# Kernel tuning notes

Hardware: AMD Instinct MI355X
Metric: run time of the kernel (lower is better)

The kernel has to match this reference:

```python
import jax, jax.numpy as jnp
import numpy as np

WS = 7            # window size
NUM_HEADS = 16
DIM = 512
B_ = 4096         # num_windows * batch
NW = 1024         # windows per image
N = WS * WS


def _relative_position_index(ws=WS):
    # static int index table, computed exactly as in the torch module
    coords = np.stack(np.meshgrid(np.arange(ws), np.arange(ws), indexing='ij'))  # (2, ws, ws)
    coords = coords.reshape(2, -1)                                               # (2, N)
    rel = coords[:, :, None] - coords[:, None, :]                                # (2, N, N)
    rel = rel.transpose(1, 2, 0).astype(np.int64)                                # (N, N, 2)
    rel[:, :, 0] += ws - 1
    rel[:, :, 1] += ws - 1
    rel[:, :, 0] *= 2 * ws - 1
    return jnp.asarray(rel.sum(-1))                                              # (N, N)


def setup_inputs() -> dict:
    key = jax.random.key(0)
    ks = jax.random.split(key, 12)
    C = DIM
    std = 0.02
    inp = {
        'local_features': jax.random.normal(ks[0], (B_, N, C), jnp.float32),
        'global_features': jax.random.normal(ks[1], (B_, N, C), jnp.float32),
        'mask': jnp.zeros((NW, N, N), jnp.float32),  # 0/-inf shifted-window mask (all-visible here)
        'bias_table': std * jax.random.normal(ks[2], ((2 * WS - 1) * (2 * WS - 1), NUM_HEADS), jnp.float32),
        'Wk': std * jax.random.normal(ks[3], (C, C), jnp.float32),
        'bk': jnp.zeros((C,), jnp.float32),
        'Wq': std * jax.random.normal(ks[4], (C, C), jnp.float32),
        'bq': jnp.zeros((C,), jnp.float32),
        'Wv': std * jax.random.normal(ks[5], (C, C), jnp.float32),
        'bv': jnp.zeros((C,), jnp.float32),
        'Wp': std * jax.random.normal(ks[6], (C, C), jnp.float32),
        'bp': jnp.zeros((C,), jnp.float32),
    }
    return inp


def reference(local_features, global_features, mask, bias_table,
              Wk, bk, Wq, bq, Wv, bv, Wp, bp):
    Bw, n, C = local_features.shape
    h = NUM_HEADS
    d = C // h
    scale = d ** -0.5

    def heads(x, W, b):
        # torch Linear: x @ W.T + b ; then (B_, N, h, d) -> (B_, h, N, d)
        y = jnp.einsum('bnc,oc->bno', x, W) + b
        return y.reshape(Bw, n, h, d).transpose(0, 2, 1, 3)

    k = heads(local_features, Wk, bk)
    q = heads(global_features, Wq, bq) * scale
    v = heads(local_features, Wv, bv)

    attn = jnp.einsum('bhnd,bhmd->bhnm', q, k)                    # (B_, h, N, N)

    idx = _relative_position_index()                               # (N, N) static
    rpb = bias_table[idx]                                          # (N, N, h)
    attn = attn + rpb.transpose(2, 0, 1)[None]                     # add (1, h, N, N)

    nW = mask.shape[0]
    attn = attn.reshape(Bw // nW, nW, h, n, n) + mask[None, :, None]
    attn = attn.reshape(Bw, h, n, n)
    attn = jax.nn.softmax(attn, axis=-1)

    x = jnp.einsum('bhnm,bhmd->bnhd', attn, v).reshape(Bw, n, C)
    x = jnp.einsum('bnc,oc->bno', x, Wp) + bp
    return x
```

## Files before the change

kernel.cpp:

```cpp
#include <hip/hip_runtime.h>
#include <hip/hip_bf16.h>

typedef __hip_bfloat16 bf16;
typedef __attribute__((ext_vector_type(4))) float f32x4;
typedef __attribute__((ext_vector_type(8))) short short8;
typedef __attribute__((ext_vector_type(4))) short short4v;

#define NEGBIG (-3.0e38f)

__device__ __forceinline__ unsigned short f2b(float x) {
  union { float f; unsigned int u; } v; v.f = x;
  unsigned int r = v.u + 0x7fffu + ((v.u >> 16) & 1u);
  return (unsigned short)(r >> 16);
}

__device__ __forceinline__ void gl16(const void* g, void* l) {
  __builtin_amdgcn_global_load_lds(
      (const __attribute__((address_space(1))) unsigned int*)g,
      (__attribute__((address_space(3))) unsigned int*)l, 16, 0, 0);
}

__device__ __forceinline__ int xcd_swz(int orig, int nwg) {
  const int q = nwg >> 3, r = nwg & 7;
  const int xcd = orig & 7;
  const int base = (xcd < r) ? xcd * (q + 1) : r * (q + 1) + (xcd - r) * q;
  return base + (orig >> 3);
}

__device__ __forceinline__ void stage32(const char* Ab, const char* Bb,
                                        char* Asb, char* Bsb, int arow0,
                                        int brow0, int k0) {
  const int tid = threadIdx.x;
#pragma unroll
  for (int i = 0; i < 2; ++i) {
    const int g = tid + 256 * i;
    const int row = g >> 2;
    const int scol = ((g & 3) ^ ((row >> 1) & 3)) << 4;
    gl16(Ab + (size_t)(arow0 + row) * 1024 + k0 * 2 + scol, Asb + g * 16);
    gl16(Bb + (size_t)(brow0 + row) * 1024 + k0 * 2 + scol, Bsb + g * 16);
  }
}

__global__ __launch_bounds__(256) void cvt_w_kernel(
    const float* __restrict__ a, const float* __restrict__ b,
    const float* __restrict__ c, const float* __restrict__ d,
    bf16* __restrict__ dst) {
  const int t = blockIdx.x * 256 + threadIdx.x;
  const float* srcs[4] = {a, b, c, d};
#pragma unroll
  for (int w = 0; w < 4; ++w) {
    const f32x4 v = *(const f32x4*)(srcs[w] + (size_t)t * 4);
    short4v o;
    o[0] = (short)f2b(v[0]); o[1] = (short)f2b(v[1]);
    o[2] = (short)f2b(v[2]); o[3] = (short)f2b(v[3]);
    *(short4v*)((short*)dst + (size_t)w * 262144 + (size_t)t * 4) = o;
  }
}

__global__ __launch_bounds__(256) void cvt_a(const float* __restrict__ src,
                                             short* __restrict__ dst, int M) {
  const int g = blockIdx.x * 256 + threadIdx.x;
  const int row = g >> 6, k8 = g & 63;
  if (row >= M) return;
  const float* sp = src + (size_t)row * 512 + k8 * 8;
  const f32x4 lo = *(const f32x4*)sp;
  const f32x4 hi = *(const f32x4*)(sp + 4);
  short8 u;
  u[0] = (short)f2b(lo[0]); u[1] = (short)f2b(lo[1]);
  u[2] = (short)f2b(lo[2]); u[3] = (short)f2b(lo[3]);
  u[4] = (short)f2b(hi[0]); u[5] = (short)f2b(hi[1]);
  u[6] = (short)f2b(hi[2]); u[7] = (short)f2b(hi[3]);
  *(short8*)(dst + (size_t)row * 512 + k8 * 8) = u;
}

__global__ __launch_bounds__(256) void prep_rpbL(const float* __restrict__ btab,
                                                 float* __restrict__ rpbL) {
  const int g = blockIdx.x * 256 + threadIdx.x;
  const int lane = g & 63, mn = (g >> 6) & 15, h = g >> 10;
  const int m = mn >> 2, n = mn & 3, l15 = lane & 15, lg = lane >> 4;
  const int cc = n * 16 + l15;
  const int aj = cc / 7, bj = cc % 7;
  f32x4 o;
#pragma unroll
  for (int reg = 0; reg < 4; ++reg) {
    const int i = m * 16 + lg * 4 + reg;
    if (i < 49 && cc < 49) {
      const int t = (i / 7 - aj + 6) * 13 + (i % 7 - bj + 6);
      o[reg] = btab[t * 16 + h];
    } else {
      o[reg] = NEGBIG;
    }
  }
  ((f32x4*)rpbL)[g] = o;
}

__global__ __launch_bounds__(256) void prep_maskL(const float* __restrict__ mask,
                                                  float* __restrict__ maskL) {
  const int g = blockIdx.x * 256 + threadIdx.x;
  const int lane = g & 63, mn = (g >> 6) & 15, wm = g >> 10;
  const int m = mn >> 2, n = mn & 3, l15 = lane & 15, lg = lane >> 4;
  const int cc = n * 16 + l15;
  f32x4 o;
#pragma unroll
  for (int reg = 0; reg < 4; ++reg) {
    const int i = m * 16 + lg * 4 + reg;
    o[reg] = (i < 49 && cc < 49) ? mask[(size_t)wm * 2401 + i * 49 + cc] : 0.f;
  }
  ((f32x4*)maskL)[g] = o;
}

__global__ __launch_bounds__(256, 4) void gemm_kqv(
    const short* __restrict__ Al, const short* __restrict__ Ag,
    const short* __restrict__ wbf, const float* __restrict__ bk,
    const float* __restrict__ bq, const float* __restrict__ bv, float qscale,
    bf16* __restrict__ k_ws, bf16* __restrict__ q_ws, bf16* __restrict__ vT_ws,
    int M) {
  __shared__ short As[8192];
  __shared__ short Bs[8192];
  const int nwg = gridDim.x;
  const int t = xcd_swz(blockIdx.x, nwg);
  const int bn = t % 12, bm = t / 12;
  const int cls = bn >> 2, bnl = bn & 3;
  const int tid = threadIdx.x, lane = tid & 63, wid = tid >> 6;
  const int wr = wid >> 1, wc = wid & 1, l15 = lane & 15, lg = lane >> 4;
  const char* Ab = (const char*)((cls == 1) ? Ag : Al);
  const char* Bb = (const char*)(wbf + (size_t)cls * 262144);

  f32x4 acc[4][4];
#pragma unroll
  for (int m = 0; m < 4; ++m)
#pragma unroll
    for (int n = 0; n < 4; ++n) acc[m][n] = (f32x4){0.f, 0.f, 0.f, 0.f};

  stage32(Ab, Bb, (char*)As, (char*)Bs, bm * 128, bnl * 128, 0);
  __syncthreads();

  for (int kt = 0; kt < 16; ++kt) {
    const int cur = kt & 1;
    if (kt < 15)
      stage32(Ab, Bb, (char*)As + (cur ^ 1) * 8192,
              (char*)Bs + (cur ^ 1) * 8192, bm * 128, bnl * 128,
              (kt + 1) * 32);
    const char* fa =
        ((cls == 2) ? (const char*)Bs : (const char*)As) + cur * 8192;
    const char* fb =
        ((cls == 2) ? (const char*)As : (const char*)Bs) + cur * 8192;
    short8 af[4], bfr[4];
#pragma unroll
    for (int m = 0; m < 4; ++m) {
      const int r = wr * 64 + m * 16 + l15;
      af[m] = *(const short8*)(fa + r * 64 +
                               ((lg << 4) ^ (((r >> 1) & 3) << 4)));
    }
#pragma unroll
    for (int n = 0; n < 4; ++n) {
      const int r = wc * 64 + n * 16 + l15;
      bfr[n] = *(const short8*)(fb + r * 64 +
                                ((lg << 4) ^ (((r >> 1) & 3) << 4)));
    }
#pragma unroll
    for (int m = 0; m < 4; ++m)
#pragma unroll
      for (int n = 0; n < 4; ++n)
        acc[m][n] = __builtin_amdgcn_mfma_f32_16x16x32_bf16(
            af[m], bfr[n], acc[m][n], 0, 0, 0);
    __syncthreads();
  }

  if (cls == 2) {
#pragma unroll
    for (int m = 0; m < 4; ++m) {
#pragma unroll
      for (int n = 0; n < 4; ++n) {
        const int tok = bm * 128 + wc * 64 + n * 16 + l15;
        if (tok < M) {
          const int w = tok / 49, nt = tok - w * 49;
#pragma unroll
          for (int reg = 0; reg < 4; ++reg) {
            const int ch = bnl * 128 + wr * 64 + m * 16 + lg * 4 + reg;
            const float v = acc[m][n][reg] + bv[ch];
            const int hh = ch >> 5, dd = ch & 31;
            vT_ws[(((size_t)w * 16 + hh) * 32 + dd) * 64 + nt] =
                __float2bfloat16(v);
          }
        }
      }
    }
  } else {
    const float* bb = (cls == 0) ? bk : bq;
    bf16* dp = (cls == 0) ? k_ws : q_ws;
    const float sc = (cls == 0) ? 1.0f : qscale;
#pragma unroll
    for (int m = 0; m < 4; ++m) {
#pragma unroll
      for (int n = 0; n < 4; ++n) {
        const int c = bnl * 128 + wc * 64 + n * 16 + l15;
        const float bvv = bb[c];
        const int hh = c >> 5, dd = c & 31;
#pragma unroll
        for (int reg = 0; reg < 4; ++reg) {
          const int r = bm * 128 + wr * 64 + m * 16 + lg * 4 + reg;
          if (r < M) {
            const int w = r / 49, nt = r - w * 49;
            dp[(((size_t)w * 16 + hh) * 49 + nt) * 32 + dd] =
                __float2bfloat16((acc[m][n][reg] + bvv) * sc);
          }
        }
      }
    }
  }
}

__global__ __launch_bounds__(256, 4) void gemm_p(const short* __restrict__ Abf,
                                                 const short* __restrict__ Bbf,
                                                 const float* __restrict__ bias,
                                                 float* __restrict__ dst,
                                                 int M) {
  __shared__ short As[8192];
  __shared__ short Bs[8192];
  const int nwg = gridDim.x;
  const int t = xcd_swz(blockIdx.x, nwg);
  const int bn = t & 3, bm = t >> 2;
  const int tid = threadIdx.x, lane = tid & 63, wid = tid >> 6;
  const int wr = wid >> 1, wc = wid & 1, l15 = lane & 15, lg = lane >> 4;
  f32x4 acc[4][4];
#pragma unroll
  for (int m = 0; m < 4; ++m)
#pragma unroll
    for (int n = 0; n < 4; ++n) acc[m][n] = (f32x4){0.f, 0.f, 0.f, 0.f};

  stage32((const char*)Abf, (const char*)Bbf, (char*)As, (char*)Bs, bm * 128,
          bn * 128, 0);
  __syncthreads();

  for (int kt = 0; kt < 16; ++kt) {
    const int cur = kt & 1;
    if (kt < 15)
      stage32((const char*)Abf, (const char*)Bbf, (char*)As + (cur ^ 1) * 8192,
              (char*)Bs + (cur ^ 1) * 8192, bm * 128, bn * 128, (kt + 1) * 32);
    const char* fa = (const char*)As + cur * 8192;
    const char* fb = (const char*)Bs + cur * 8192;
    short8 af[4], bfr[4];
#pragma unroll
    for (int m = 0; m < 4; ++m) {
      const int r = wr * 64 + m * 16 + l15;
      af[m] = *(const short8*)(fa + r * 64 +
                               ((lg << 4) ^ (((r >> 1) & 3) << 4)));
    }
#pragma unroll
    for (int n = 0; n < 4; ++n) {
      const int r = wc * 64 + n * 16 + l15;
      bfr[n] = *(const short8*)(fb + r * 64 +
                                ((lg << 4) ^ (((r >> 1) & 3) << 4)));
    }
#pragma unroll
    for (int m = 0; m < 4; ++m)
#pragma unroll
      for (int n = 0; n < 4; ++n)
        acc[m][n] = __builtin_amdgcn_mfma_f32_16x16x32_bf16(
            af[m], bfr[n], acc[m][n], 0, 0, 0);
    __syncthreads();
  }
#pragma unroll
  for (int m = 0; m < 4; ++m) {
#pragma unroll
    for (int n = 0; n < 4; ++n) {
      const int c = bn * 128 + wc * 64 + n * 16 + l15;
      const float bvv = bias[c];
#pragma unroll
      for (int reg = 0; reg < 4; ++reg) {
        const int r = bm * 128 + wr * 64 + m * 16 + lg * 4 + reg;
        if (r < M) dst[(size_t)r * 512 + c] = acc[m][n][reg] + bvv;
      }
    }
  }
}

__global__ __launch_bounds__(256) void attn_win2(
    const bf16* __restrict__ q_ws, const bf16* __restrict__ k_ws,
    const bf16* __restrict__ vT_ws, const float* __restrict__ rpbL,
    const float* __restrict__ maskL, bf16* __restrict__ x_ws, int wstart) {
  __shared__ short sP[4][4096];
  const int tid = threadIdx.x, lane = tid & 63, wid = tid >> 6;
  const int l15 = lane & 15, lg = lane >> 4;
  const int wl = blockIdx.x;
  const int h = blockIdx.y * 4 + wid;
  const int wg = wstart + wl;
  char* Pl = (char*)sP[wid];
  const size_t base = ((size_t)wl * 16 + h) * 1568;
  const short8 z8 = (short8){0, 0, 0, 0, 0, 0, 0, 0};

  short8 qf[4], kf[4];
#pragma unroll
  for (int m = 0; m < 4; ++m) {
    const int r = m * 16 + l15;
    qf[m] = (r < 49) ? *(const short8*)(q_ws + base + r * 32 + lg * 8) : z8;
    kf[m] = (r < 49) ? *(const short8*)(k_ws + base + r * 32 + lg * 8) : z8;
  }
  f32x4 lc[4][4];
#pragma unroll
  for (int m = 0; m < 4; ++m)
#pragma unroll
    for (int n = 0; n < 4; ++n)
      lc[m][n] = __builtin_amdgcn_mfma_f32_16x16x32_bf16(
          qf[m], kf[n], (f32x4){0.f, 0.f, 0.f, 0.f}, 0, 0, 0);

  const f32x4* rbp = (const f32x4*)rpbL + (size_t)h * 1024 + lane;
  const f32x4* mkp = (const f32x4*)maskL + (size_t)(wg & 1023) * 1024 + lane;
#pragma unroll
  for (int m = 0; m < 4; ++m)
#pragma unroll
    for (int n = 0; n < 4; ++n) {
      const int mn = m * 4 + n;
      lc[m][n] += rbp[mn * 64] + mkp[mn * 64];
    }

#pragma unroll
  for (int m = 0; m < 4; ++m) {
#pragma unroll
    for (int reg = 0; reg < 4; ++reg) {
      float vmax = fmaxf(fmaxf(lc[m][0][reg], lc[m][1][reg]),
                         fmaxf(lc[m][2][reg], lc[m][3][reg]));
#pragma unroll
      for (int off = 1; off < 16; off <<= 1)
        vmax = fmaxf(vmax, __shfl_xor(vmax, off, 64));
      float e[4], ssum = 0.f;
#pragma unroll
      for (int n = 0; n < 4; ++n) {
        e[n] = __expf(lc[m][n][reg] - vmax);
        ssum += e[n];
      }
#pragma unroll
      for (int off = 1; off < 16; off <<= 1) ssum += __shfl_xor(ssum, off, 64);
      const float inv = __builtin_amdgcn_rcpf(ssum);
      const int i = m * 16 + lg * 4 + reg;
#pragma unroll
      for (int n = 0; n < 4; ++n) {
        const int cc = n * 16 + l15;
        *(unsigned short*)(Pl + i * 128 + ((2 * cc) ^ ((i & 7) << 4))) =
            f2b(e[n] * inv);
      }
    }
  }

  f32x4 xacc[4][2];
#pragma unroll
  for (int m = 0; m < 4; ++m)
#pragma unroll
    for (int n = 0; n < 2; ++n) xacc[m][n] = (f32x4){0.f, 0.f, 0.f, 0.f};
  const size_t vbase = ((size_t)wl * 16 + h) * 2048;
#pragma unroll
  for (int s = 0; s < 2; ++s) {
    short8 pf[4], vf[2];
#pragma unroll
    for (int m = 0; m < 4; ++m) {
      const int i = m * 16 + l15;
      pf[m] = *(const short8*)(Pl + i * 128 +
                               ((s * 64 + lg * 16) ^ ((i & 7) << 4)));
    }
#pragma unroll
    for (int n = 0; n < 2; ++n) {
      const int dd = n * 16 + l15;
      short8 vv = *(const short8*)(vT_ws + vbase + dd * 64 + s * 32 + lg * 8);
      if (s == 1) {
        if (lg == 3) vv = z8;
        else if (lg == 2) {
          vv[1] = 0; vv[2] = 0; vv[3] = 0; vv[4] = 0;
          vv[5] = 0; vv[6] = 0; vv[7] = 0;
        }
      }
      vf[n] = vv;
    }
#pragma unroll
    for (int m = 0; m < 4; ++m)
#pragma unroll
      for (int n = 0; n < 2; ++n)
        xacc[m][n] = __builtin_amdgcn_mfma_f32_16x16x32_bf16(
            pf[m], vf[n], xacc[m][n], 0, 0, 0);
  }

#pragma unroll
  for (int m = 0; m < 4; ++m)
#pragma unroll
    for (int n = 0; n < 2; ++n)
#pragma unroll
      for (int reg = 0; reg < 4; ++reg) {
        const int i = m * 16 + lg * 4 + reg;
        const int dd = n * 16 + l15;
        *(unsigned short*)(Pl + i * 80 + ((2 * dd) ^ ((i & 3) << 4))) =
            f2b(xacc[m][n][reg]);
      }
#pragma unroll
  for (int g = 0; g < 4; ++g) {
    const int row = g * 16 + (lane >> 2);
    if (row < 49) {
      const short8 xv = *(const short8*)(
          Pl + row * 80 + (((lane & 3) * 16) ^ ((row & 3) << 4)));
      *(short8*)(x_ws + ((size_t)wl * 49 + row) * 512 + h * 32 +
                 (lane & 3) * 8) = xv;
    }
  }
}

extern "C" void kernel_launch(void* const* d_in, const int* in_sizes, int n_in,
                              void* d_out, int out_size, void* d_ws,
                              size_t ws_size, hipStream_t stream) {
  const float* lf   = (const float*)d_in[0];
  const float* gfx  = (const float*)d_in[1];
  const float* mask = (const float*)d_in[2];
  const float* btab = (const float*)d_in[3];
  const float* Wk = (const float*)d_in[4];  const float* bk = (const float*)d_in[5];
  const float* Wq = (const float*)d_in[6];  const float* bq = (const float*)d_in[7];
  const float* Wv = (const float*)d_in[8];  const float* bv = (const float*)d_in[9];
  const float* Wp = (const float*)d_in[10]; const float* bp = (const float*)d_in[11];
  float* out = (float*)d_out;

  char* ws = (char*)d_ws;
  short* wbf = (short*)ws;
  size_t off = (size_t)4 * 262144 * 2;
  float* rpbL = (float*)(ws + off); off += (size_t)16 * 4096 * 4;
  float* maskL = (float*)(ws + off); off += (size_t)1024 * 4096 * 4;

  const size_t perw = 2 * 49 * 1024 + 2 * 50176 + 65536;
  size_t avail = (ws_size > off + 65536) ? ws_size - off - 65536 : 0;
  int CH = (int)((avail > 300000) ? (avail - 262144) / perw : 1);
  if (CH > 4096) CH = 4096;
  if (CH < 1) CH = 1;
  const int RWS = ((CH * 49 + 127) / 128) * 128;

  short* Al = (short*)(ws + off); off += (size_t)RWS * 1024;
  short* Ag = (short*)(ws + off); off += (size_t)RWS * 1024;
  bf16* q_ws = (bf16*)(ws + off); off += (size_t)CH * 50176;
  bf16* k_ws = (bf16*)(ws + off); off += (size_t)CH * 50176;
  bf16* vT_ws = (bf16*)(ws + off); off += (size_t)CH * 65536;
  bf16* x_ws = (bf16*)Al;

  cvt_w_kernel<<<256, 256, 0, stream>>>(Wk, Wq, Wv, Wp, (bf16*)wbf);
  prep_rpbL<<<64, 256, 0, stream>>>(btab, rpbL);
  prep_maskL<<<4096, 256, 0, stream>>>(mask, maskL);

  const float qscale = 0.17677669529663687f;
  for (int wstart = 0; wstart < 4096; wstart += CH) {
    const int nwin = (4096 - wstart < CH) ? (4096 - wstart) : CH;
    const int M = nwin * 49;
    const int gy = (M + 127) / 128;
    const int cg = (M * 64 + 255) / 256;
    cvt_a<<<cg, 256, 0, stream>>>(lf + (size_t)wstart * 25088, Al, M);
    cvt_a<<<cg, 256, 0, stream>>>(gfx + (size_t)wstart * 25088, Ag, M);
    gemm_kqv<<<12 * gy, 256, 0, stream>>>(Al, Ag, wbf, bk, bq, bv, qscale,
                                          k_ws, q_ws, vT_ws, M);
    attn_win2<<<dim3(nwin, 4), 256, 0, stream>>>(q_ws, k_ws, vT_ws, rpbL,
                                                 maskL, x_ws, wstart);
    gemm_p<<<4 * gy, 256, 0, stream>>>((const short*)x_ws, wbf + 3 * 262144,
                                       bp, out + (size_t)wstart * 25088, M);
  }
}
```

Before: 1.326 ms.

## Fuse fp32-to-bf16 activation conversion into KQV GEMM with triple-buffered LDS pipeline

```diff
diff --git a/kernel.cpp b/kernel.cpp
--- a/kernel.cpp
+++ b/kernel.cpp
@@ -25,20 +25,6 @@
   const int xcd = orig & 7;
   const int base = (xcd < r) ? xcd * (q + 1) : r * (q + 1) + (xcd - r) * q;
   return base + (orig >> 3);
-}
-
-__device__ __forceinline__ void stage32(const char* Ab, const char* Bb,
-                                        char* Asb, char* Bsb, int arow0,
-                                        int brow0, int k0) {
-  const int tid = threadIdx.x;
-#pragma unroll
-  for (int i = 0; i < 2; ++i) {
-    const int g = tid + 256 * i;
-    const int row = g >> 2;
-    const int scol = ((g & 3) ^ ((row >> 1) & 3)) << 4;
-    gl16(Ab + (size_t)(arow0 + row) * 1024 + k0 * 2 + scol, Asb + g * 16);
-    gl16(Bb + (size_t)(brow0 + row) * 1024 + k0 * 2 + scol, Bsb + g * 16);
-  }
 }
 
 __global__ __launch_bounds__(256) void cvt_w_kernel(
@@ -55,22 +41,6 @@
     o[2] = (short)f2b(v[2]); o[3] = (short)f2b(v[3]);
     *(short4v*)((short*)dst + (size_t)w * 262144 + (size_t)t * 4) = o;
   }
-}
-
-__global__ __launch_bounds__(256) void cvt_a(const float* __restrict__ src,
-                                             short* __restrict__ dst, int M) {
-  const int g = blockIdx.x * 256 + threadIdx.x;
-  const int row = g >> 6, k8 = g & 63;
-  if (row >= M) return;
-  const float* sp = src + (size_t)row * 512 + k8 * 8;
-  const f32x4 lo = *(const f32x4*)sp;
-  const f32x4 hi = *(const f32x4*)(sp + 4);
-  short8 u;
-  u[0] = (short)f2b(lo[0]); u[1] = (short)f2b(lo[1]);
-  u[2] = (short)f2b(lo[2]); u[3] = (short)f2b(lo[3]);
-  u[4] = (short)f2b(hi[0]); u[5] = (short)f2b(hi[1]);
-  u[6] = (short)f2b(hi[2]); u[7] = (short)f2b(hi[3]);
-  *(short8*)(dst + (size_t)row * 512 + k8 * 8) = u;
 }
 
 __global__ __launch_bounds__(256) void prep_rpbL(const float* __restrict__ btab,
@@ -109,22 +79,71 @@
   ((f32x4*)maskL)[g] = o;
 }
 
-__global__ __launch_bounds__(256, 4) void gemm_kqv(
-    const short* __restrict__ Al, const short* __restrict__ Ag,
+__global__ __launch_bounds__(256, 3) void gemm_kqv(
+    const float* __restrict__ Alf, const float* __restrict__ Agf,
     const short* __restrict__ wbf, const float* __restrict__ bk,
     const float* __restrict__ bq, const float* __restrict__ bv, float qscale,
     bf16* __restrict__ k_ws, bf16* __restrict__ q_ws, bf16* __restrict__ vT_ws,
     int M) {
-  __shared__ short As[8192];
-  __shared__ short Bs[8192];
+  __shared__ char lds[49152];
   const int nwg = gridDim.x;
-  const int t = xcd_swz(blockIdx.x, nwg);
-  const int bn = t % 12, bm = t / 12;
+  const int t0 = xcd_swz(blockIdx.x, nwg);
+  const int bn = t0 % 12, bm = t0 / 12;
   const int cls = bn >> 2, bnl = bn & 3;
   const int tid = threadIdx.x, lane = tid & 63, wid = tid >> 6;
   const int wr = wid >> 1, wc = wid & 1, l15 = lane & 15, lg = lane >> 4;
-  const char* Ab = (const char*)((cls == 1) ? Ag : Al);
+  const float* Af = (cls == 1) ? Agf : Alf;
   const char* Bb = (const char*)(wbf + (size_t)cls * 262144);
+  const bool swap = (cls == 2);
+
+  const int gS0 = tid, gS1 = tid + 256;
+  const int rowS0 = gS0 >> 2, rowS1 = gS1 >> 2;
+  const int c4S0 = (gS0 & 3) ^ ((rowS0 >> 1) & 3);
+  const int c4S1 = (gS1 & 3) ^ ((rowS1 >> 1) & 3);
+  const int gr0 = bm * 128 + rowS0, gr1 = bm * 128 + rowS1;
+  const bool v0 = gr0 < M, v1 = gr1 < M;
+  const float* ap0 = Af + (size_t)gr0 * 512 + c4S0 * 8;
+  const float* ap1 = Af + (size_t)gr1 * 512 + c4S1 * 8;
+  const char* bp0 = Bb + (size_t)(bnl * 128 + rowS0) * 1024 + c4S0 * 16;
+  const char* bp1 = Bb + (size_t)(bnl * 128 + rowS1) * 1024 + c4S1 * 16;
+
+  f32x4 a00 = (f32x4){0.f, 0.f, 0.f, 0.f}, a01 = a00, a10 = a00, a11 = a00;
+
+#define ISSUE_A(k0)                                                       \
+  do {                                                                    \
+    if (v0) {                                                             \
+      a00 = *(const f32x4*)(ap0 + (k0));                                  \
+      a01 = *(const f32x4*)(ap0 + (k0) + 4);                              \
+    }                                                                     \
+    if (v1) {                                                             \
+      a10 = *(const f32x4*)(ap1 + (k0));                                  \
+      a11 = *(const f32x4*)(ap1 + (k0) + 4);                              \
+    }                                                                     \
+  } while (0)
+#define ISSUE_B(buf, k0)                                                  \
+  do {                                                                    \
+    gl16(bp0 + (size_t)(k0) * 2, (buf) + 8192 + gS0 * 16);                \
+    gl16(bp1 + (size_t)(k0) * 2, (buf) + 8192 + gS1 * 16);                \
+  } while (0)
+#define WRITE_A(buf)                                                      \
+  do {                                                                    \
+    if (v0) {                                                             \
+      short8 u;                                                           \
+      u[0] = (short)f2b(a00[0]); u[1] = (short)f2b(a00[1]);               \
+      u[2] = (short)f2b(a00[2]); u[3] = (short)f2b(a00[3]);               \
+      u[4] = (short)f2b(a01[0]); u[5] = (short)f2b(a01[1]);               \
+      u[6] = (short)f2b(a01[2]); u[7] = (short)f2b(a01[3]);               \
+      *(short8*)((buf) + gS0 * 16) = u;                                   \
+    }                                                                     \
+    if (v1) {                                                             \
+      short8 u;                                                           \
+      u[0] = (short)f2b(a10[0]); u[1] = (short)f2b(a10[1]);               \
+      u[2] = (short)f2b(a10[2]); u[3] = (short)f2b(a10[3]);               \
+      u[4] = (short)f2b(a11[0]); u[5] = (short)f2b(a11[1]);               \
+      u[6] = (short)f2b(a11[2]); u[7] = (short)f2b(a11[3]);               \
+      *(short8*)((buf) + gS1 * 16) = u;                                   \
+    }                                                                     \
+  } while (0)
 
   f32x4 acc[4][4];
 #pragma unroll
@@ -132,40 +151,52 @@
 #pragma unroll
     for (int n = 0; n < 4; ++n) acc[m][n] = (f32x4){0.f, 0.f, 0.f, 0.f};
 
-  stage32(Ab, Bb, (char*)As, (char*)Bs, bm * 128, bnl * 128, 0);
-  __syncthreads();
-
-  for (int kt = 0; kt < 16; ++kt) {
-    const int cur = kt & 1;
-    if (kt < 15)
-      stage32(Ab, Bb, (char*)As + (cur ^ 1) * 8192,
-              (char*)Bs + (cur ^ 1) * 8192, bm * 128, bnl * 128,
-              (kt + 1) * 32);
-    const char* fa =
-        ((cls == 2) ? (const char*)Bs : (const char*)As) + cur * 8192;
-    const char* fb =
-        ((cls == 2) ? (const char*)As : (const char*)Bs) + cur * 8192;
+  ISSUE_A(0); ISSUE_B(lds, 0); WRITE_A(lds);
+  ISSUE_A(32); ISSUE_B(lds + 16384, 32); WRITE_A(lds + 16384);
+  asm volatile("s_waitcnt vmcnt(2) lgkmcnt(0)" ::: "memory");
+  __builtin_amdgcn_s_barrier();
+  __builtin_amdgcn_sched_barrier(0);
+
+#pragma unroll 1
+  for (int t = 0; t < 16; ++t) {
+    char* cbuf = lds + (t % 3) * 16384;
+    char* sbuf = lds + ((t + 2) % 3) * 16384;
+    if (t < 14) { ISSUE_A((t + 2) * 32); ISSUE_B(sbuf, (t + 2) * 32); }
+    const char* fa = swap ? cbuf + 8192 : cbuf;
+    const char* fb = swap ? cbuf : cbuf + 8192;
     short8 af[4], bfr[4];
 #pragma unroll
     for (int m = 0; m < 4; ++m) {
       const int r = wr * 64 + m * 16 + l15;
-      af[m] = *(const short8*)(fa + r * 64 +
-                               ((lg << 4) ^ (((r >> 1) & 3) << 4)));
+      af[m] = *(const short8*)(fa + r * 64 + ((lg ^ ((r >> 1) & 3)) << 4));
     }
 #pragma unroll
     for (int n = 0; n < 4; ++n) {
       const int r = wc * 64 + n * 16 + l15;
-      bfr[n] = *(const short8*)(fb + r * 64 +
-                                ((lg << 4) ^ (((r >> 1) & 3) << 4)));
-    }
+      bfr[n] = *(const short8*)(fb + r * 64 + ((lg ^ ((r >> 1) & 3)) << 4));
+    }
+    __builtin_amdgcn_s_setprio(1);
 #pragma unroll
     for (int m = 0; m < 4; ++m)
 #pragma unroll
       for (int n = 0; n < 4; ++n)
         acc[m][n] = __builtin_amdgcn_mfma_f32_16x16x32_bf16(
             af[m], bfr[n], acc[m][n], 0, 0, 0);
-    __syncthreads();
-  }
+    __builtin_amdgcn_s_setprio(0);
+    if (t < 14) WRITE_A(sbuf);
+    if (t < 14) {
+      asm volatile("s_waitcnt vmcnt(2) lgkmcnt(0)" ::: "memory");
+    } else if (t == 14) {
+      asm volatile("s_waitcnt vmcnt(0) lgkmcnt(0)" ::: "memory");
+    }
+    if (t < 15) {
+      __builtin_amdgcn_s_barrier();
+      __builtin_amdgcn_sched_barrier(0);
+    }
+  }
+#undef ISSUE_A
+#undef ISSUE_B
+#undef WRITE_A
 
   if (cls == 2) {
 #pragma unroll
@@ -211,56 +242,86 @@
   }
 }
 
-__global__ __launch_bounds__(256, 4) void gemm_p(const short* __restrict__ Abf,
+__global__ __launch_bounds__(256, 3) void gemm_p(const short* __restrict__ Abf,
                                                  const short* __restrict__ Bbf,
                                                  const float* __restrict__ bias,
                                                  float* __restrict__ dst,
                                                  int M) {
-  __shared__ short As[8192];
-  __shared__ short Bs[8192];
+  __shared__ char lds[49152];
   const int nwg = gridDim.x;
-  const int t = xcd_swz(blockIdx.x, nwg);
-  const int bn = t & 3, bm = t >> 2;
+  const int t0 = xcd_swz(blockIdx.x, nwg);
+  const int bn = t0 & 3, bm = t0 >> 2;
   const int tid = threadIdx.x, lane = tid & 63, wid = tid >> 6;
   const int wr = wid >> 1, wc = wid & 1, l15 = lane & 15, lg = lane >> 4;
+
+  const int gS0 = tid, gS1 = tid + 256;
+  const int rowS0 = gS0 >> 2, rowS1 = gS1 >> 2;
+  const int c4S0 = (gS0 & 3) ^ ((rowS0 >> 1) & 3);
+  const int c4S1 = (gS1 & 3) ^ ((rowS1 >> 1) & 3);
+  const char* Ab = (const char*)Abf;
+  const char* Bb = (const char*)Bbf;
+  const char* ap0 = Ab + (size_t)(bm * 128 + rowS0) * 1024 + c4S0 * 16;
+  const char* ap1 = Ab + (size_t)(bm * 128 + rowS1) * 1024 + c4S1 * 16;
+  const char* bp0 = Bb + (size_t)(bn * 128 + rowS0) * 1024 + c4S0 * 16;
+  const char* bp1 = Bb + (size_t)(bn * 128 + rowS1) * 1024 + c4S1 * 16;
+
+#define STAGE_P(buf, k0)                                                  \
+  do {                                                                    \
+    gl16(ap0 + (size_t)(k0) * 2, (buf) + gS0 * 16);                       \
+    gl16(ap1 + (size_t)(k0) * 2, (buf) + gS1 * 16);                       \
+    gl16(bp0 + (size_t)(k0) * 2, (buf) + 8192 + gS0 * 16);                \
+    gl16(bp1 + (size_t)(k0) * 2, (buf) + 8192 + gS1 * 16);                \
+  } while (0)
+
   f32x4 acc[4][4];
 #pragma unroll
   for (int m = 0; m < 4; ++m)
 #pragma unroll
     for (int n = 0; n < 4; ++n) acc[m][n] = (f32x4){0.f, 0.f, 0.f, 0.f};
 
-  stage32((const char*)Abf, (const char*)Bbf, (char*)As, (char*)Bs, bm * 128,
-          bn * 128, 0);
-  __syncthreads();
-
-  for (int kt = 0; kt < 16; ++kt) {
-    const int cur = kt & 1;
-    if (kt < 15)
-      stage32((const char*)Abf, (const char*)Bbf, (char*)As + (cur ^ 1) * 8192,
-              (char*)Bs + (cur ^ 1) * 8192, bm * 128, bn * 128, (kt + 1) * 32);
-    const char* fa = (const char*)As + cur * 8192;
-    const char* fb = (const char*)Bs + cur * 8192;
+  STAGE_P(lds, 0);
+  STAGE_P(lds + 16384, 32);
+  asm volatile("s_waitcnt vmcnt(4)" ::: "memory");
+  __builtin_amdgcn_s_barrier();
+  __builtin_amdgcn_sched_barrier(0);
+
+#pragma unroll 1
+  for (int t = 0; t < 16; ++t) {
+    char* cbuf = lds + (t % 3) * 16384;
+    char* sbuf = lds + ((t + 2) % 3) * 16384;
+    if (t < 14) STAGE_P(sbuf, (t + 2) * 32);
     short8 af[4], bfr[4];
 #pragma unroll
     for (int m = 0; m < 4; ++m) {
       const int r = wr * 64 + m * 16 + l15;
-      af[m] = *(const short8*)(fa + r * 64 +
-                               ((lg << 4) ^ (((r >> 1) & 3) << 4)));
+      af[m] = *(const short8*)(cbuf + r * 64 + ((lg ^ ((r >> 1) & 3)) << 4));
     }
 #pragma unroll
     for (int n = 0; n < 4; ++n) {
       const int r = wc * 64 + n * 16 + l15;
-      bfr[n] = *(const short8*)(fb + r * 64 +
-                                ((lg << 4) ^ (((r >> 1) & 3) << 4)));
-    }
+      bfr[n] =
+          *(const short8*)(cbuf + 8192 + r * 64 + ((lg ^ ((r >> 1) & 3)) << 4));
+    }
+    __builtin_amdgcn_s_setprio(1);
 #pragma unroll
     for (int m = 0; m < 4; ++m)
 #pragma unroll
       for (int n = 0; n < 4; ++n)
         acc[m][n] = __builtin_amdgcn_mfma_f32_16x16x32_bf16(
             af[m], bfr[n], acc[m][n], 0, 0, 0);
-    __syncthreads();
-  }
+    __builtin_amdgcn_s_setprio(0);
+    if (t < 14) {
+      asm volatile("s_waitcnt vmcnt(4)" ::: "memory");
+    } else if (t == 14) {
+      asm volatile("s_waitcnt vmcnt(0)" ::: "memory");
+    }
+    if (t < 15) {
+      __builtin_amdgcn_s_barrier();
+      __builtin_amdgcn_sched_barrier(0);
+    }
+  }
+#undef STAGE_P
+
 #pragma unroll
   for (int m = 0; m < 4; ++m) {
 #pragma unroll
@@ -421,19 +482,16 @@
   float* rpbL = (float*)(ws + off); off += (size_t)16 * 4096 * 4;
   float* maskL = (float*)(ws + off); off += (size_t)1024 * 4096 * 4;
 
-  const size_t perw = 2 * 49 * 1024 + 2 * 50176 + 65536;
+  const size_t perw = 3 * 50176 + 65536;
   size_t avail = (ws_size > off + 65536) ? ws_size - off - 65536 : 0;
-  int CH = (int)((avail > 300000) ? (avail - 262144) / perw : 1);
+  int CH = (int)(avail / perw);
   if (CH > 4096) CH = 4096;
   if (CH < 1) CH = 1;
-  const int RWS = ((CH * 49 + 127) / 128) * 128;
-
-  short* Al = (short*)(ws + off); off += (size_t)RWS * 1024;
-  short* Ag = (short*)(ws + off); off += (size_t)RWS * 1024;
+
+  bf16* x_ws = (bf16*)(ws + off); off += (size_t)CH * 50176;
   bf16* q_ws = (bf16*)(ws + off); off += (size_t)CH * 50176;
   bf16* k_ws = (bf16*)(ws + off); off += (size_t)CH * 50176;
   bf16* vT_ws = (bf16*)(ws + off); off += (size_t)CH * 65536;
-  bf16* x_ws = (bf16*)Al;
 
   cvt_w_kernel<<<256, 256, 0, stream>>>(Wk, Wq, Wv, Wp, (bf16*)wbf);
   prep_rpbL<<<64, 256, 0, stream>>>(btab, rpbL);
@@ -444,11 +502,10 @@
     const int nwin = (4096 - wstart < CH) ? (4096 - wstart) : CH;
     const int M = nwin * 49;
     const int gy = (M + 127) / 128;
-    const int cg = (M * 64 + 255) / 256;
-    cvt_a<<<cg, 256, 0, stream>>>(lf + (size_t)wstart * 25088, Al, M);
-    cvt_a<<<cg, 256, 0, stream>>>(gfx + (size_t)wstart * 25088, Ag, M);
-    gemm_kqv<<<12 * gy, 256, 0, stream>>>(Al, Ag, wbf, bk, bq, bv, qscale,
-                                          k_ws, q_ws, vT_ws, M);
+    gemm_kqv<<<12 * gy, 256, 0, stream>>>(lf + (size_t)wstart * 25088,
+                                          gfx + (size_t)wstart * 25088, wbf,
+                                          bk, bq, bv, qscale, k_ws, q_ws,
+                                          vT_ws, M);
     attn_win2<<<dim3(nwin, 4), 256, 0, stream>>>(q_ws, k_ws, vT_ws, rpbL,
                                                  maskL, x_ws, wstart);
     gemm_p<<<4 * gy, 256, 0, stream>>>((const short*)x_ws, wbf + 3 * 262144,
```

New measurement: 1.544 ms. 1.16x slower.
